# Performance work log

Measured on AMD Instinct MI355X. Metric: run time of the kernel, lower is better.

## Reference

```python
import jax, jax.numpy as jnp
import numpy as np

N = 100000
C_IN, C_OUT = 128, 64
BN_EPS = 1e-5
SLOPE = 0.01  # torch LeakyReLU default


def setup_inputs() -> dict:
    key = jax.random.key(0)
    ks = jax.random.split(key, 12)

    def w(k, K, cin, cout):
        return jax.random.normal(k, (K, cin, cout), jnp.float32) / np.sqrt(K * cin)

    x_feats = jax.random.normal(ks[0], (N, C_IN), jnp.float32)
    skip_feats = jax.random.normal(ks[1], (N, C_OUT), jnp.float32)
    W1 = w(ks[2], 27, C_IN, C_OUT)
    Wt = w(ks[3], 27, C_OUT, C_OUT)
    W2 = w(ks[4], 9, C_OUT, C_OUT)
    W3 = w(ks[5], 9, C_OUT, C_OUT)
    W4 = w(ks[6], 27, C_OUT, C_OUT)
    # bn[l] = (gamma, beta, running_mean, running_var) for BN layer l
    gamma = 1.0 + 0.01 * jax.random.normal(ks[7], (4, C_OUT), jnp.float32)
    beta = 0.01 * jax.random.normal(ks[8], (4, C_OUT), jnp.float32)
    mean = 0.1 * jax.random.normal(ks[9], (4, C_OUT), jnp.float32)
    var = jax.random.uniform(ks[10], (4, C_OUT), jnp.float32, 0.5, 1.5)
    bn = jnp.stack([gamma, beta, mean, var], axis=1)  # [4, 4, C_OUT]

    nk = jax.random.split(ks[11], 5)
    nbr1 = jax.random.randint(nk[0], (27, N), 0, N, jnp.int64)
    nbrt = jax.random.randint(nk[1], (27, N), 0, N, jnp.int64)
    nbr2 = jax.random.randint(nk[2], (9, N), 0, N, jnp.int64)
    nbr3 = jax.random.randint(nk[3], (9, N), 0, N, jnp.int64)
    nbr4 = jax.random.randint(nk[4], (27, N), 0, N, jnp.int64)
    return dict(x_feats=x_feats, skip_feats=skip_feats, W1=W1, Wt=Wt, W2=W2,
                W3=W3, W4=W4, bn=bn, nbr1=nbr1, nbrt=nbrt, nbr2=nbr2,
                nbr3=nbr3, nbr4=nbr4)


def sparse_conv(feats, W, nbr):
    """Gather-GEMM-accumulate sparse conv.

    feats: [N, Cin]; W: [K, Cin, Cout]; nbr: [K, N] neighbor index per tap.
    out[i] = sum_k feats[nbr[k, i]] @ W[k]
    """
    acc0 = jnp.zeros((feats.shape[0], W.shape[-1]), feats.dtype)

    def step(acc, wn):
        w_k, idx_k = wn
        return acc + feats[idx_k] @ w_k, None

    out, _ = jax.lax.scan(step, acc0, (W, nbr))
    return out


def bn_lrelu(x, p):
    gamma, beta, mean, var = p[0], p[1], p[2], p[3]
    y = (x - mean) * jax.lax.rsqrt(var + BN_EPS) * gamma + beta
    return jnp.where(y >= 0, y, SLOPE * y)


def reference(x_feats, skip_feats, W1, Wt, W2, W3, W4, bn,
              nbr1, nbrt, nbr2, nbr3, nbr4):
    # up_block: conv3x3x3 + BN + LeakyReLU, then transposed conv (no BN/act)
    h = bn_lrelu(sparse_conv(x_feats, W1, nbr1), bn[0])
    h = sparse_conv(h, Wt, nbrt)
    h = h + skip_feats  # out.feats += skip.feats
    # conv_x3: three conv blocks
    h = bn_lrelu(sparse_conv(h, W2, nbr2), bn[1])
    h = bn_lrelu(sparse_conv(h, W3, nbr3), bn[2])
    h = bn_lrelu(sparse_conv(h, W4, nbr4), bn[3])
    return h
```

## Files before the change

kernel.cpp:

```cpp
#include <hip/hip_runtime.h>
#include <stdint.h>


typedef __bf16 bf16x8 __attribute__((ext_vector_type(8)));
typedef float f32x16 __attribute__((ext_vector_type(16)));

__device__ __forceinline__ uint16_t f2bf(float f) {
    uint32_t u = __builtin_bit_cast(uint32_t, f);
    u = (u + 0x7fffu + ((u >> 16) & 1u)) >> 16;
    return (uint16_t)u;
}

__device__ __forceinline__ bf16x8 ldb8(const uint16_t* p) {
    return __builtin_bit_cast(bf16x8, *reinterpret_cast<const uint4*>(p));
}

__global__ void convert_x(const float* __restrict__ in, uint16_t* __restrict__ out, int n8) {
    int t = blockIdx.x * blockDim.x + threadIdx.x;
    if (t >= n8) return;
    const float4* p = reinterpret_cast<const float4*>(in) + 2 * (size_t)t;
    float4 f0 = p[0], f1 = p[1];
    uint32_t w0 = (uint32_t)f2bf(f0.x) | ((uint32_t)f2bf(f0.y) << 16);
    uint32_t w1 = (uint32_t)f2bf(f0.z) | ((uint32_t)f2bf(f0.w) << 16);
    uint32_t w2 = (uint32_t)f2bf(f1.x) | ((uint32_t)f2bf(f1.y) << 16);
    uint32_t w3 = (uint32_t)f2bf(f1.z) | ((uint32_t)f2bf(f1.w) << 16);
    uint4 v; v.x = w0; v.y = w1; v.z = w2; v.w = w3;
    *reinterpret_cast<uint4*>(out + 8 * (size_t)t) = v;
}

__global__ void pack_weights(const float* __restrict__ w1, const float* __restrict__ wt,
                             const float* __restrict__ w2, const float* __restrict__ w3,
                             const float* __restrict__ w4, const float* __restrict__ bn,
                             uint16_t* __restrict__ p1, uint16_t* __restrict__ pt,
                             uint16_t* __restrict__ p2, uint16_t* __restrict__ p3,
                             uint16_t* __restrict__ p4, float* __restrict__ bnps) {
    int w = blockIdx.y;
    int t = blockIdx.x * blockDim.x + threadIdx.x;
    if (w == 5) {
        if (t < 256) {
            int l = t >> 6, c = t & 63;
            float g = bn[(l * 4 + 0) * 64 + c];
            float b = bn[(l * 4 + 1) * 64 + c];
            float m = bn[(l * 4 + 2) * 64 + c];
            float v = bn[(l * 4 + 3) * 64 + c];
            float sc = g * rsqrtf(v + 1e-5f);
            bnps[(l * 2 + 0) * 64 + c] = sc;
            bnps[(l * 2 + 1) * 64 + c] = b - m * sc;
        }
        return;
    }
    const float* src; uint16_t* dst; int K, CIN;
    switch (w) {
        case 0:  src = w1; dst = p1; K = 27; CIN = 128; break;
        case 1:  src = wt; dst = pt; K = 27; CIN = 64;  break;
        case 2:  src = w2; dst = p2; K = 9;  CIN = 64;  break;
        case 3:  src = w3; dst = p3; K = 9;  CIN = 64;  break;
        default: src = w4; dst = p4; K = 27; CIN = 64;  break;
    }
    int S = CIN / 16;
    int F = K * S * 2 * 64;
    if (t >= F) return;
    int lane = t & 63;
    int r = t >> 6;
    int nt = r & 1; r >>= 1;
    int s = r % S;
    int k = r / S;
    int c = nt * 32 + (lane & 31);
    int cib = s * 16 + (lane >> 5) * 8;
    #pragma unroll
    for (int j = 0; j < 8; ++j)
        dst[(size_t)t * 8 + j] = f2bf(src[((size_t)k * CIN + cib + j) * 64 + c]);
}

template <int CIN, int MODE>
__global__ __launch_bounds__(64)
void conv_layer(const uint16_t* __restrict__ feats,
                const uint16_t* __restrict__ wf,
                const int* __restrict__ nbr,
                const int K, const int npts,
                const float* __restrict__ bnp,
                const float* __restrict__ skip,
                uint16_t* __restrict__ outb,
                float* __restrict__ outf) {
    constexpr int S = CIN / 16;
    const int lane = threadIdx.x;
    const int l31  = lane & 31;
    const int hi   = lane >> 5;
    const int base = blockIdx.x * 64;
    const int r0 = base + l31;
    const int r1 = r0 + 32;
    const int g0 = min(r0, npts - 1);
    const int g1 = min(r1, npts - 1);

    f32x16 acc00 = {0,0,0,0,0,0,0,0,0,0,0,0,0,0,0,0};
    f32x16 acc01 = {0,0,0,0,0,0,0,0,0,0,0,0,0,0,0,0};
    f32x16 acc10 = {0,0,0,0,0,0,0,0,0,0,0,0,0,0,0,0};
    f32x16 acc11 = {0,0,0,0,0,0,0,0,0,0,0,0,0,0,0,0};

    for (int k = 0; k < K; ++k) {
        const int i0 = nbr[(size_t)k * npts + g0];
        const int i1 = nbr[(size_t)k * npts + g1];
        const uint16_t* a0p = feats + (size_t)i0 * CIN + hi * 8;
        const uint16_t* a1p = feats + (size_t)i1 * CIN + hi * 8;
        const uint16_t* bp  = wf + (size_t)k * (S * 1024) + lane * 8;
        #pragma unroll
        for (int s = 0; s < S; ++s) {
            bf16x8 a0 = ldb8(a0p + s * 16);
            bf16x8 a1 = ldb8(a1p + s * 16);
            bf16x8 b0 = ldb8(bp + s * 1024);
            bf16x8 b1 = ldb8(bp + s * 1024 + 512);
            acc00 = __builtin_amdgcn_mfma_f32_32x32x16_bf16(a0, b0, acc00, 0, 0, 0);
            acc01 = __builtin_amdgcn_mfma_f32_32x32x16_bf16(a0, b1, acc01, 0, 0, 0);
            acc10 = __builtin_amdgcn_mfma_f32_32x32x16_bf16(a1, b0, acc10, 0, 0, 0);
            acc11 = __builtin_amdgcn_mfma_f32_32x32x16_bf16(a1, b1, acc11, 0, 0, 0);
        }
    }

    const int c0 = l31, c1 = 32 + l31;
    float sc0 = 0.f, sh0 = 0.f, sc1 = 0.f, sh1 = 0.f;
    if (MODE != 1) {
        sc0 = bnp[c0]; sh0 = bnp[64 + c0];
        sc1 = bnp[c1]; sh1 = bnp[64 + c1];
    }
    #pragma unroll
    for (int reg = 0; reg < 16; ++reg) {
        const int row = (reg & 3) + 8 * (reg >> 2) + 4 * hi;
        const int gr0 = base + row;
        const int gr1 = base + 32 + row;
        float v00 = acc00[reg], v01 = acc01[reg];
        float v10 = acc10[reg], v11 = acc11[reg];
        if (MODE != 1) {
            v00 = v00 * sc0 + sh0; v00 = v00 >= 0.f ? v00 : 0.01f * v00;
            v01 = v01 * sc1 + sh1; v01 = v01 >= 0.f ? v01 : 0.01f * v01;
            v10 = v10 * sc0 + sh0; v10 = v10 >= 0.f ? v10 : 0.01f * v10;
            v11 = v11 * sc1 + sh1; v11 = v11 >= 0.f ? v11 : 0.01f * v11;
        }
        if (gr0 < npts) {
            if (MODE == 1) { v00 += skip[(size_t)gr0 * 64 + c0]; v01 += skip[(size_t)gr0 * 64 + c1]; }
            if (MODE == 2) {
                outf[(size_t)gr0 * 64 + c0] = v00; outf[(size_t)gr0 * 64 + c1] = v01;
            } else {
                outb[(size_t)gr0 * 64 + c0] = f2bf(v00); outb[(size_t)gr0 * 64 + c1] = f2bf(v01);
            }
        }
        if (gr1 < npts) {
            if (MODE == 1) { v10 += skip[(size_t)gr1 * 64 + c0]; v11 += skip[(size_t)gr1 * 64 + c1]; }
            if (MODE == 2) {
                outf[(size_t)gr1 * 64 + c0] = v10; outf[(size_t)gr1 * 64 + c1] = v11;
            } else {
                outb[(size_t)gr1 * 64 + c0] = f2bf(v10); outb[(size_t)gr1 * 64 + c1] = f2bf(v11);
            }
        }
    }
}

extern "C" void kernel_launch(void* const* d_in, const int* in_sizes, int n_in,
                              void* d_out, int out_size, void* d_ws, size_t ws_size,
                              hipStream_t stream) {
    const int N = in_sizes[0] / 128;
    const float* x    = (const float*)d_in[0];
    const float* skip = (const float*)d_in[1];
    const float* W1   = (const float*)d_in[2];
    const float* Wt   = (const float*)d_in[3];
    const float* W2   = (const float*)d_in[4];
    const float* W3   = (const float*)d_in[5];
    const float* W4   = (const float*)d_in[6];
    const float* bn   = (const float*)d_in[7];
    const int* nbr1   = (const int*)d_in[8];
    const int* nbrt   = (const int*)d_in[9];
    const int* nbr2   = (const int*)d_in[10];
    const int* nbr3   = (const int*)d_in[11];
    const int* nbr4   = (const int*)d_in[12];

    uint8_t* ws = (uint8_t*)d_ws;
    size_t off = 0;
    auto carve = [&](size_t bytes) -> void* {
        void* p = ws + off;
        off += (bytes + 255) & ~(size_t)255;
        return p;
    };
    uint16_t* xb  = (uint16_t*)carve((size_t)N * 128 * 2);
    uint16_t* hA  = (uint16_t*)carve((size_t)N * 64 * 2);
    uint16_t* hB  = (uint16_t*)carve((size_t)N * 64 * 2);
    uint16_t* p1  = (uint16_t*)carve((size_t)27 * 128 * 64 * 2);
    uint16_t* pt  = (uint16_t*)carve((size_t)27 * 64 * 64 * 2);
    uint16_t* p2  = (uint16_t*)carve((size_t)9 * 64 * 64 * 2);
    uint16_t* p3  = (uint16_t*)carve((size_t)9 * 64 * 64 * 2);
    uint16_t* p4  = (uint16_t*)carve((size_t)27 * 64 * 64 * 2);
    float*    bnp = (float*)carve((size_t)4 * 2 * 64 * 4);

    const int n8 = N * 16;
    convert_x<<<(n8 + 255) / 256, 256, 0, stream>>>(x, xb, n8);
    pack_weights<<<dim3(108, 6), 256, 0, stream>>>(W1, Wt, W2, W3, W4, bn,
                                                   p1, pt, p2, p3, p4, bnp);

    const int grid = (N + 63) / 64;
    conv_layer<128, 0><<<grid, 64, 0, stream>>>(xb, p1, nbr1, 27, N, bnp + 0,   nullptr, hA, nullptr);
    conv_layer<64,  1><<<grid, 64, 0, stream>>>(hA, pt, nbrt, 27, N, nullptr,   skip,    hB, nullptr);
    conv_layer<64,  0><<<grid, 64, 0, stream>>>(hB, p2, nbr2, 9,  N, bnp + 128, nullptr, hA, nullptr);
    conv_layer<64,  0><<<grid, 64, 0, stream>>>(hA, p3, nbr3, 9,  N, bnp + 256, nullptr, hB, nullptr);
    conv_layer<64,  2><<<grid, 64, 0, stream>>>(hB, p4, nbr4, 27, N, bnp + 384, nullptr, nullptr, (float*)d_out);
}
```

Before: 536.4 us.

## Split conv tiles to 32 rows per wave, 4 waves per block, prefetch neighbor indices

Each wave now computes a 32-row by 64-channel tile instead of 64 rows, with four waves packed into a 256-thread block, halving accumulator registers and doubling wave count. The tap count K becomes a template parameter, so all neighbor indices for the row are loaded up front into registers before the MFMA loop, taking the index load latency off the per-tap path. In exchange, each weight fragment is reused across half as many rows, so weight-load traffic per output roughly doubles. The larger index array also raises register pressure for K=27.

After: 557.7 us. 1.04x slower.

```diff
diff --git a/kernel.cpp b/kernel.cpp
--- a/kernel.cpp
+++ b/kernel.cpp
@@ -72,47 +72,42 @@
         dst[(size_t)t * 8 + j] = f2bf(src[((size_t)k * CIN + cib + j) * 64 + c]);
 }
 
-template <int CIN, int MODE>
-__global__ __launch_bounds__(64)
+template <int CIN, int K, int MODE>
+__global__ __launch_bounds__(256)
 void conv_layer(const uint16_t* __restrict__ feats,
                 const uint16_t* __restrict__ wf,
                 const int* __restrict__ nbr,
-                const int K, const int npts,
+                const int npts,
                 const float* __restrict__ bnp,
                 const float* __restrict__ skip,
                 uint16_t* __restrict__ outb,
                 float* __restrict__ outf) {
     constexpr int S = CIN / 16;
-    const int lane = threadIdx.x;
+    const int lane = threadIdx.x & 63;
+    const int wave = threadIdx.x >> 6;
     const int l31  = lane & 31;
     const int hi   = lane >> 5;
-    const int base = blockIdx.x * 64;
-    const int r0 = base + l31;
-    const int r1 = r0 + 32;
-    const int g0 = min(r0, npts - 1);
-    const int g1 = min(r1, npts - 1);
+    const int base = (blockIdx.x * 4 + wave) * 32;
+    const int g    = min(base + l31, npts - 1);
 
-    f32x16 acc00 = {0,0,0,0,0,0,0,0,0,0,0,0,0,0,0,0};
-    f32x16 acc01 = {0,0,0,0,0,0,0,0,0,0,0,0,0,0,0,0};
-    f32x16 acc10 = {0,0,0,0,0,0,0,0,0,0,0,0,0,0,0,0};
-    f32x16 acc11 = {0,0,0,0,0,0,0,0,0,0,0,0,0,0,0,0};
+    int idx[K];
+    #pragma unroll
+    for (int k = 0; k < K; ++k) idx[k] = nbr[(size_t)k * npts + g];
 
+    f32x16 acc0 = {0,0,0,0,0,0,0,0,0,0,0,0,0,0,0,0};
+    f32x16 acc1 = {0,0,0,0,0,0,0,0,0,0,0,0,0,0,0,0};
+
+    #pragma unroll 3
     for (int k = 0; k < K; ++k) {
-        const int i0 = nbr[(size_t)k * npts + g0];
-        const int i1 = nbr[(size_t)k * npts + g1];
-        const uint16_t* a0p = feats + (size_t)i0 * CIN + hi * 8;
-        const uint16_t* a1p = feats + (size_t)i1 * CIN + hi * 8;
-        const uint16_t* bp  = wf + (size_t)k * (S * 1024) + lane * 8;
+        const uint16_t* ap = feats + (size_t)idx[k] * CIN + hi * 8;
+        const uint16_t* bp = wf + (size_t)k * (S * 1024) + lane * 8;
         #pragma unroll
         for (int s = 0; s < S; ++s) {
-            bf16x8 a0 = ldb8(a0p + s * 16);
-            bf16x8 a1 = ldb8(a1p + s * 16);
+            bf16x8 a  = ldb8(ap + s * 16);
             bf16x8 b0 = ldb8(bp + s * 1024);
             bf16x8 b1 = ldb8(bp + s * 1024 + 512);
-            acc00 = __builtin_amdgcn_mfma_f32_32x32x16_bf16(a0, b0, acc00, 0, 0, 0);
-            acc01 = __builtin_amdgcn_mfma_f32_32x32x16_bf16(a0, b1, acc01, 0, 0, 0);
-            acc10 = __builtin_amdgcn_mfma_f32_32x32x16_bf16(a1, b0, acc10, 0, 0, 0);
-            acc11 = __builtin_amdgcn_mfma_f32_32x32x16_bf16(a1, b1, acc11, 0, 0, 0);
+            acc0 = __builtin_amdgcn_mfma_f32_32x32x16_bf16(a, b0, acc0, 0, 0, 0);
+            acc1 = __builtin_amdgcn_mfma_f32_32x32x16_bf16(a, b1, acc1, 0, 0, 0);
         }
     }
 
@@ -125,31 +120,22 @@
     #pragma unroll
     for (int reg = 0; reg < 16; ++reg) {
         const int row = (reg & 3) + 8 * (reg >> 2) + 4 * hi;
-        const int gr0 = base + row;
-        const int gr1 = base + 32 + row;
-        float v00 = acc00[reg], v01 = acc01[reg];
-        float v10 = acc10[reg], v11 = acc11[reg];
+        const int gr = base + row;
+        if (gr >= npts) continue;
+        float v0 = acc0[reg], v1 = acc1[reg];
         if (MODE != 1) {
-            v00 = v00 * sc0 + sh0; v00 = v00 >= 0.f ? v00 : 0.01f * v00;
-            v01 = v01 * sc1 + sh1; v01 = v01 >= 0.f ? v01 : 0.01f * v01;
-            v10 = v10 * sc0 + sh0; v10 = v10 >= 0.f ? v10 : 0.01f * v10;
-            v11 = v11 * sc1 + sh1; v11 = v11 >= 0.f ? v11 : 0.01f * v11;
+            v0 = v0 * sc0 + sh0; v0 = v0 >= 0.f ? v0 : 0.01f * v0;
+            v1 = v1 * sc1 + sh1; v1 = v1 >= 0.f ? v1 : 0.01f * v1;
+        } else {
+            v0 += skip[(size_t)gr * 64 + c0];
+            v1 += skip[(size_t)gr * 64 + c1];
         }
-        if (gr0 < npts) {
-            if (MODE == 1) { v00 += skip[(size_t)gr0 * 64 + c0]; v01 += skip[(size_t)gr0 * 64 + c1]; }
-            if (MODE == 2) {
-                outf[(size_t)gr0 * 64 + c0] = v00; outf[(size_t)gr0 * 64 + c1] = v01;
-            } else {
-                outb[(size_t)gr0 * 64 + c0] = f2bf(v00); outb[(size_t)gr0 * 64 + c1] = f2bf(v01);
-            }
-        }
-        if (gr1 < npts) {
-            if (MODE == 1) { v10 += skip[(size_t)gr1 * 64 + c0]; v11 += skip[(size_t)gr1 * 64 + c1]; }
-            if (MODE == 2) {
-                outf[(size_t)gr1 * 64 + c0] = v10; outf[(size_t)gr1 * 64 + c1] = v11;
-            } else {
-                outb[(size_t)gr1 * 64 + c0] = f2bf(v10); outb[(size_t)gr1 * 64 + c1] = f2bf(v11);
-            }
+        if (MODE == 2) {
+            outf[(size_t)gr * 64 + c0] = v0;
+            outf[(size_t)gr * 64 + c1] = v1;
+        } else {
+            outb[(size_t)gr * 64 + c0] = f2bf(v0);
+            outb[(size_t)gr * 64 + c1] = f2bf(v1);
         }
     }
 }
@@ -194,10 +180,10 @@
     pack_weights<<<dim3(108, 6), 256, 0, stream>>>(W1, Wt, W2, W3, W4, bn,
                                                    p1, pt, p2, p3, p4, bnp);
 
-    const int grid = (N + 63) / 64;
-    conv_layer<128, 0><<<grid, 64, 0, stream>>>(xb, p1, nbr1, 27, N, bnp + 0,   nullptr, hA, nullptr);
-    conv_layer<64,  1><<<grid, 64, 0, stream>>>(hA, pt, nbrt, 27, N, nullptr,   skip,    hB, nullptr);
-    conv_layer<64,  0><<<grid, 64, 0, stream>>>(hB, p2, nbr2, 9,  N, bnp + 128, nullptr, hA, nullptr);
-    conv_layer<64,  0><<<grid, 64, 0, stream>>>(hA, p3, nbr3, 9,  N, bnp + 256, nullptr, hB, nullptr);
-    conv_layer<64,  2><<<grid, 64, 0, stream>>>(hB, p4, nbr4, 27, N, bnp + 384, nullptr, nullptr, (float*)d_out);
+    const int grid = (N + 127) / 128;
+    conv_layer<128, 27, 0><<<grid, 256, 0, stream>>>(xb, p1, nbr1, N, bnp + 0,   nullptr, hA, nullptr);
+    conv_layer<64,  27, 1><<<grid, 256, 0, stream>>>(hA, pt, nbrt, N, nullptr,   skip,    hB, nullptr);
+    conv_layer<64,  9,  0><<<grid, 256, 0, stream>>>(hB, p2, nbr2, N, bnp + 128, nullptr, hA, nullptr);
+    conv_layer<64,  9,  0><<<grid, 256, 0, stream>>>(hA, p3, nbr3, N, bnp + 256, nullptr, hB, nullptr);
+    conv_layer<64,  27, 2><<<grid, 256, 0, stream>>>(hB, p4, nbr4, N, bnp + 384, nullptr, nullptr, (float*)d_out);
 }
```

## Fuse conversion, packing and five conv layers into one cooperative kernel

Applied to the files above, without the earlier changes.

Merges the input conversion, weight packing and all five sparse conv layers into a single cooperative kernel, with a grid-wide sync between stages. Each block loops over tiles with a grid stride. The goal is to remove the per-kernel launch gaps and the tail drain between the seven separate launches. In exchange it adds grid-sync cost, and the fused kernel may need more registers, which could lower occupancy or make the cooperative launch fail. If the launch fails, it falls back to the original multi-kernel path.

New measurement: 1.739 ms. 224% more time.

```diff
diff --git a/kernel.cpp b/kernel.cpp
--- a/kernel.cpp
+++ b/kernel.cpp
@@ -1,5 +1,8 @@
 #include <hip/hip_runtime.h>
+#include <hip/hip_cooperative_groups.h>
 #include <stdint.h>
+
+namespace cg = cooperative_groups;
 
 
 typedef __bf16 bf16x8 __attribute__((ext_vector_type(8)));
@@ -15,9 +18,9 @@
     return __builtin_bit_cast(bf16x8, *reinterpret_cast<const uint4*>(p));
 }
 
-__global__ void convert_x(const float* __restrict__ in, uint16_t* __restrict__ out, int n8) {
-    int t = blockIdx.x * blockDim.x + threadIdx.x;
-    if (t >= n8) return;
+
+__device__ __forceinline__ void convert_body(const float* __restrict__ in,
+                                             uint16_t* __restrict__ out, int t) {
     const float4* p = reinterpret_cast<const float4*>(in) + 2 * (size_t)t;
     float4 f0 = p[0], f1 = p[1];
     uint32_t w0 = (uint32_t)f2bf(f0.x) | ((uint32_t)f2bf(f0.y) << 16);
@@ -28,65 +31,47 @@
     *reinterpret_cast<uint4*>(out + 8 * (size_t)t) = v;
 }
 
-__global__ void pack_weights(const float* __restrict__ w1, const float* __restrict__ wt,
-                             const float* __restrict__ w2, const float* __restrict__ w3,
-                             const float* __restrict__ w4, const float* __restrict__ bn,
-                             uint16_t* __restrict__ p1, uint16_t* __restrict__ pt,
-                             uint16_t* __restrict__ p2, uint16_t* __restrict__ p3,
-                             uint16_t* __restrict__ p4, float* __restrict__ bnps) {
-    int w = blockIdx.y;
-    int t = blockIdx.x * blockDim.x + threadIdx.x;
-    if (w == 5) {
-        if (t < 256) {
-            int l = t >> 6, c = t & 63;
-            float g = bn[(l * 4 + 0) * 64 + c];
-            float b = bn[(l * 4 + 1) * 64 + c];
-            float m = bn[(l * 4 + 2) * 64 + c];
-            float v = bn[(l * 4 + 3) * 64 + c];
-            float sc = g * rsqrtf(v + 1e-5f);
-            bnps[(l * 2 + 0) * 64 + c] = sc;
-            bnps[(l * 2 + 1) * 64 + c] = b - m * sc;
-        }
-        return;
-    }
-    const float* src; uint16_t* dst; int K, CIN;
-    switch (w) {
-        case 0:  src = w1; dst = p1; K = 27; CIN = 128; break;
-        case 1:  src = wt; dst = pt; K = 27; CIN = 64;  break;
-        case 2:  src = w2; dst = p2; K = 9;  CIN = 64;  break;
-        case 3:  src = w3; dst = p3; K = 9;  CIN = 64;  break;
-        default: src = w4; dst = p4; K = 27; CIN = 64;  break;
-    }
+__device__ __forceinline__ void pack_body(const float* __restrict__ src,
+                                          uint16_t* __restrict__ dst,
+                                          int CIN, int t) {
     int S = CIN / 16;
-    int F = K * S * 2 * 64;
-    if (t >= F) return;
-    int lane = t & 63;
+    int l = t & 63;
     int r = t >> 6;
     int nt = r & 1; r >>= 1;
     int s = r % S;
     int k = r / S;
-    int c = nt * 32 + (lane & 31);
-    int cib = s * 16 + (lane >> 5) * 8;
+    int c = nt * 32 + (l & 31);
+    int cib = s * 16 + (l >> 5) * 8;
     #pragma unroll
     for (int j = 0; j < 8; ++j)
         dst[(size_t)t * 8 + j] = f2bf(src[((size_t)k * CIN + cib + j) * 64 + c]);
 }
 
+__device__ __forceinline__ void bn_body(const float* __restrict__ bn,
+                                        float* __restrict__ bnps, int t) {
+    int l = t >> 6, c = t & 63;
+    float g = bn[(l * 4 + 0) * 64 + c];
+    float b = bn[(l * 4 + 1) * 64 + c];
+    float m = bn[(l * 4 + 2) * 64 + c];
+    float v = bn[(l * 4 + 3) * 64 + c];
+    float sc = g * rsqrtf(v + 1e-5f);
+    bnps[(l * 2 + 0) * 64 + c] = sc;
+    bnps[(l * 2 + 1) * 64 + c] = b - m * sc;
+}
+
 template <int CIN, int MODE>
-__global__ __launch_bounds__(64)
-void conv_layer(const uint16_t* __restrict__ feats,
-                const uint16_t* __restrict__ wf,
-                const int* __restrict__ nbr,
-                const int K, const int npts,
-                const float* __restrict__ bnp,
-                const float* __restrict__ skip,
-                uint16_t* __restrict__ outb,
-                float* __restrict__ outf) {
+__device__ void conv_tile(int base, int lane,
+                          const uint16_t* __restrict__ feats,
+                          const uint16_t* __restrict__ wf,
+                          const int* __restrict__ nbr,
+                          const int K, const int npts,
+                          const float* __restrict__ bnp,
+                          const float* __restrict__ skip,
+                          uint16_t* __restrict__ outb,
+                          float* __restrict__ outf) {
     constexpr int S = CIN / 16;
-    const int lane = threadIdx.x;
-    const int l31  = lane & 31;
-    const int hi   = lane >> 5;
-    const int base = blockIdx.x * 64;
+    const int l31 = lane & 31;
+    const int hi  = lane >> 5;
     const int r0 = base + l31;
     const int r1 = r0 + 32;
     const int g0 = min(r0, npts - 1);
@@ -154,23 +139,85 @@
     }
 }
 
+struct UPParams {
+    const float* x; const float* skip;
+    const float* W1; const float* Wt; const float* W2; const float* W3; const float* W4;
+    const float* bn;
+    const int* nbr1; const int* nbrt; const int* nbr2; const int* nbr3; const int* nbr4;
+    uint16_t* xb; uint16_t* hA; uint16_t* hB;
+    uint16_t* p1; uint16_t* pt; uint16_t* p2; uint16_t* p3; uint16_t* p4;
+    float* bnp; float* out;
+    int N; int n8; int ntiles;
+};
+
+__global__ __launch_bounds__(64)
+void fused_upblock(UPParams P) {
+    cg::grid_group grid = cg::this_grid();
+    const int lane = threadIdx.x;
+    const int gthreads = gridDim.x * 64;
+    const int gt0 = blockIdx.x * 64 + lane;
+
+    for (int t = gt0; t < P.n8; t += gthreads) convert_body(P.x, P.xb, t);
+    for (int t = gt0; t < 27 * 8 * 2 * 64; t += gthreads) pack_body(P.W1, P.p1, 128, t);
+    for (int t = gt0; t < 27 * 4 * 2 * 64; t += gthreads) pack_body(P.Wt, P.pt, 64, t);
+    for (int t = gt0; t < 9 * 4 * 2 * 64;  t += gthreads) pack_body(P.W2, P.p2, 64, t);
+    for (int t = gt0; t < 9 * 4 * 2 * 64;  t += gthreads) pack_body(P.W3, P.p3, 64, t);
+    for (int t = gt0; t < 27 * 4 * 2 * 64; t += gthreads) pack_body(P.W4, P.p4, 64, t);
+    for (int t = gt0; t < 256; t += gthreads) bn_body(P.bn, P.bnp, t);
+
+    __threadfence(); grid.sync(); __threadfence();
+
+    for (int tile = blockIdx.x; tile < P.ntiles; tile += gridDim.x)
+        conv_tile<128, 0>(tile * 64, lane, P.xb, P.p1, P.nbr1, 27, P.N, P.bnp, nullptr, P.hA, nullptr);
+    __threadfence(); grid.sync(); __threadfence();
+
+    for (int tile = blockIdx.x; tile < P.ntiles; tile += gridDim.x)
+        conv_tile<64, 1>(tile * 64, lane, P.hA, P.pt, P.nbrt, 27, P.N, nullptr, P.skip, P.hB, nullptr);
+    __threadfence(); grid.sync(); __threadfence();
+
+    for (int tile = blockIdx.x; tile < P.ntiles; tile += gridDim.x)
+        conv_tile<64, 0>(tile * 64, lane, P.hB, P.p2, P.nbr2, 9, P.N, P.bnp + 128, nullptr, P.hA, nullptr);
+    __threadfence(); grid.sync(); __threadfence();
+
+    for (int tile = blockIdx.x; tile < P.ntiles; tile += gridDim.x)
+        conv_tile<64, 0>(tile * 64, lane, P.hA, P.p3, P.nbr3, 9, P.N, P.bnp + 256, nullptr, P.hB, nullptr);
+    __threadfence(); grid.sync(); __threadfence();
+
+    for (int tile = blockIdx.x; tile < P.ntiles; tile += gridDim.x)
+        conv_tile<64, 2>(tile * 64, lane, P.hB, P.p4, P.nbr4, 27, P.N, P.bnp + 384, nullptr, nullptr, P.out);
+}
+
+__global__ void convert_x_g(const float* __restrict__ in, uint16_t* __restrict__ out, int n8) {
+    int t = blockIdx.x * blockDim.x + threadIdx.x;
+    if (t < n8) convert_body(in, out, t);
+}
+
+__global__ void pack_weights_g(UPParams P) {
+    int w = blockIdx.y;
+    int t = blockIdx.x * blockDim.x + threadIdx.x;
+    switch (w) {
+        case 0: if (t < 27 * 8 * 2 * 64) pack_body(P.W1, P.p1, 128, t); break;
+        case 1: if (t < 27 * 4 * 2 * 64) pack_body(P.Wt, P.pt, 64, t); break;
+        case 2: if (t < 9 * 4 * 2 * 64)  pack_body(P.W2, P.p2, 64, t); break;
+        case 3: if (t < 9 * 4 * 2 * 64)  pack_body(P.W3, P.p3, 64, t); break;
+        case 4: if (t < 27 * 4 * 2 * 64) pack_body(P.W4, P.p4, 64, t); break;
+        default: if (t < 256) bn_body(P.bn, P.bnp, t); break;
+    }
+}
+
+template <int CIN, int MODE>
+__global__ __launch_bounds__(64)
+void conv_layer_g(const uint16_t* __restrict__ feats, const uint16_t* __restrict__ wf,
+                  const int* __restrict__ nbr, const int K, const int npts,
+                  const float* __restrict__ bnp, const float* __restrict__ skip,
+                  uint16_t* __restrict__ outb, float* __restrict__ outf) {
+    conv_tile<CIN, MODE>(blockIdx.x * 64, threadIdx.x, feats, wf, nbr, K, npts, bnp, skip, outb, outf);
+}
+
 extern "C" void kernel_launch(void* const* d_in, const int* in_sizes, int n_in,
                               void* d_out, int out_size, void* d_ws, size_t ws_size,
                               hipStream_t stream) {
     const int N = in_sizes[0] / 128;
-    const float* x    = (const float*)d_in[0];
-    const float* skip = (const float*)d_in[1];
-    const float* W1   = (const float*)d_in[2];
-    const float* Wt   = (const float*)d_in[3];
-    const float* W2   = (const float*)d_in[4];
-    const float* W3   = (const float*)d_in[5];
-    const float* W4   = (const float*)d_in[6];
-    const float* bn   = (const float*)d_in[7];
-    const int* nbr1   = (const int*)d_in[8];
-    const int* nbrt   = (const int*)d_in[9];
-    const int* nbr2   = (const int*)d_in[10];
-    const int* nbr3   = (const int*)d_in[11];
-    const int* nbr4   = (const int*)d_in[12];
 
     uint8_t* ws = (uint8_t*)d_ws;
     size_t off = 0;
@@ -179,25 +226,47 @@
         off += (bytes + 255) & ~(size_t)255;
         return p;
     };
-    uint16_t* xb  = (uint16_t*)carve((size_t)N * 128 * 2);
-    uint16_t* hA  = (uint16_t*)carve((size_t)N * 64 * 2);
-    uint16_t* hB  = (uint16_t*)carve((size_t)N * 64 * 2);
-    uint16_t* p1  = (uint16_t*)carve((size_t)27 * 128 * 64 * 2);
-    uint16_t* pt  = (uint16_t*)carve((size_t)27 * 64 * 64 * 2);
-    uint16_t* p2  = (uint16_t*)carve((size_t)9 * 64 * 64 * 2);
-    uint16_t* p3  = (uint16_t*)carve((size_t)9 * 64 * 64 * 2);
-    uint16_t* p4  = (uint16_t*)carve((size_t)27 * 64 * 64 * 2);
-    float*    bnp = (float*)carve((size_t)4 * 2 * 64 * 4);
-
-    const int n8 = N * 16;
-    convert_x<<<(n8 + 255) / 256, 256, 0, stream>>>(x, xb, n8);
-    pack_weights<<<dim3(108, 6), 256, 0, stream>>>(W1, Wt, W2, W3, W4, bn,
-                                                   p1, pt, p2, p3, p4, bnp);
-
-    const int grid = (N + 63) / 64;
-    conv_layer<128, 0><<<grid, 64, 0, stream>>>(xb, p1, nbr1, 27, N, bnp + 0,   nullptr, hA, nullptr);
-    conv_layer<64,  1><<<grid, 64, 0, stream>>>(hA, pt, nbrt, 27, N, nullptr,   skip,    hB, nullptr);
-    conv_layer<64,  0><<<grid, 64, 0, stream>>>(hB, p2, nbr2, 9,  N, bnp + 128, nullptr, hA, nullptr);
-    conv_layer<64,  0><<<grid, 64, 0, stream>>>(hA, p3, nbr3, 9,  N, bnp + 256, nullptr, hB, nullptr);
-    conv_layer<64,  2><<<grid, 64, 0, stream>>>(hB, p4, nbr4, 27, N, bnp + 384, nullptr, nullptr, (float*)d_out);
-}
+
+    UPParams P;
+    P.x    = (const float*)d_in[0];
+    P.skip = (const float*)d_in[1];
+    P.W1   = (const float*)d_in[2];
+    P.Wt   = (const float*)d_in[3];
+    P.W2   = (const float*)d_in[4];
+    P.W3   = (const float*)d_in[5];
+    P.W4   = (const float*)d_in[6];
+    P.bn   = (const float*)d_in[7];
+    P.nbr1 = (const int*)d_in[8];
+    P.nbrt = (const int*)d_in[9];
+    P.nbr2 = (const int*)d_in[10];
+    P.nbr3 = (const int*)d_in[11];
+    P.nbr4 = (const int*)d_in[12];
+    P.xb   = (uint16_t*)carve((size_t)N * 128 * 2);
+    P.hA   = (uint16_t*)carve((size_t)N * 64 * 2);
+    P.hB   = (uint16_t*)carve((size_t)N * 64 * 2);
+    P.p1   = (uint16_t*)carve((size_t)27 * 128 * 64 * 2);
+    P.pt   = (uint16_t*)carve((size_t)27 * 64 * 64 * 2);
+    P.p2   = (uint16_t*)carve((size_t)9 * 64 * 64 * 2);
+    P.p3   = (uint16_t*)carve((size_t)9 * 64 * 64 * 2);
+    P.p4   = (uint16_t*)carve((size_t)27 * 64 * 64 * 2);
+    P.bnp  = (float*)carve((size_t)4 * 2 * 64 * 4);
+    P.out  = (float*)d_out;
+    P.N = N;
+    P.n8 = N * 16;
+    P.ntiles = (N + 63) / 64;
+
+    void* kargs[] = { (void*)&P };
+    hipError_t err = hipLaunchCooperativeKernel((const void*)fused_upblock,
+                                                dim3(P.ntiles), dim3(64),
+                                                kargs, 0, stream);
+    if (err != hipSuccess) {
+        convert_x_g<<<(P.n8 + 255) / 256, 256, 0, stream>>>(P.x, P.xb, P.n8);
+        pack_weights_g<<<dim3(108, 6), 256, 0, stream>>>(P);
+        const int grid = P.ntiles;
+        conv_layer_g<128, 0><<<grid, 64, 0, stream>>>(P.xb, P.p1, P.nbr1, 27, N, P.bnp,       nullptr, P.hA, nullptr);
+        conv_layer_g<64,  1><<<grid, 64, 0, stream>>>(P.hA, P.pt, P.nbrt, 27, N, nullptr,     P.skip,  P.hB, nullptr);
+        conv_layer_g<64,  0><<<grid, 64, 0, stream>>>(P.hB, P.p2, P.nbr2, 9,  N, P.bnp + 128, nullptr, P.hA, nullptr);
+        conv_layer_g<64,  0><<<grid, 64, 0, stream>>>(P.hA, P.p3, P.nbr3, 9,  N, P.bnp + 256, nullptr, P.hB, nullptr);
+        conv_layer_g<64,  2><<<grid, 64, 0, stream>>>(P.hB, P.p4, P.nbr4, 27, N, P.bnp + 384, nullptr, nullptr, P.out);
+    }
+}
```

## Stage conv weights in LDS shared by four waves per block

Applied to the files above, without the earlier changes.

Each block now runs four waves, each computing 64 output rows, and cooperatively copies chunks of taps' packed weights into 64KB of shared memory. The waves then read B fragments from LDS instead of global memory. This cuts redundant weight traffic through L2/L1 and makes K a compile-time constant so the tap loops can unroll. In exchange it adds barriers per chunk and uses a large LDS footprint, which can limit blocks per CU and reduce occupancy for this gather-latency-bound kernel.

New measurement: 548.3 us. +2.2%, slower.

```diff
diff --git a/kernel.cpp b/kernel.cpp
--- a/kernel.cpp
+++ b/kernel.cpp
@@ -72,48 +72,74 @@
         dst[(size_t)t * 8 + j] = f2bf(src[((size_t)k * CIN + cib + j) * 64 + c]);
 }
 
-template <int CIN, int MODE>
-__global__ __launch_bounds__(64)
+template <int CIN, int K, int MODE>
+__global__ __launch_bounds__(256)
 void conv_layer(const uint16_t* __restrict__ feats,
                 const uint16_t* __restrict__ wf,
                 const int* __restrict__ nbr,
-                const int K, const int npts,
+                const int npts,
                 const float* __restrict__ bnp,
                 const float* __restrict__ skip,
                 uint16_t* __restrict__ outb,
                 float* __restrict__ outf) {
     constexpr int S = CIN / 16;
-    const int lane = threadIdx.x;
+    constexpr int C = 32 / S;
+    constexpr int NFULL = K / C;
+    constexpr int REM = K % C;
+
+    __shared__ uint16_t Bs[32768];
+
+    const int lane = threadIdx.x & 63;
+    const int wave = threadIdx.x >> 6;
     const int l31  = lane & 31;
     const int hi   = lane >> 5;
-    const int base = blockIdx.x * 64;
-    const int r0 = base + l31;
-    const int r1 = r0 + 32;
-    const int g0 = min(r0, npts - 1);
-    const int g1 = min(r1, npts - 1);
+    const int base = (blockIdx.x * 4 + wave) * 64;
+    const int g0   = min(base + l31, npts - 1);
+    const int g1   = min(base + 32 + l31, npts - 1);
 
     f32x16 acc00 = {0,0,0,0,0,0,0,0,0,0,0,0,0,0,0,0};
     f32x16 acc01 = {0,0,0,0,0,0,0,0,0,0,0,0,0,0,0,0};
     f32x16 acc10 = {0,0,0,0,0,0,0,0,0,0,0,0,0,0,0,0};
     f32x16 acc11 = {0,0,0,0,0,0,0,0,0,0,0,0,0,0,0,0};
 
-    for (int k = 0; k < K; ++k) {
+    auto stage = [&](int k0, int units) {
+        const uint4* gsrc = reinterpret_cast<const uint4*>(wf + (size_t)k0 * (S * 1024));
+        uint4* dst = reinterpret_cast<uint4*>(Bs);
+        for (int u = threadIdx.x; u < units; u += 256) dst[u] = gsrc[u];
+    };
+
+    auto do_tap = [&](int k, int kk) {
         const int i0 = nbr[(size_t)k * npts + g0];
         const int i1 = nbr[(size_t)k * npts + g1];
         const uint16_t* a0p = feats + (size_t)i0 * CIN + hi * 8;
         const uint16_t* a1p = feats + (size_t)i1 * CIN + hi * 8;
-        const uint16_t* bp  = wf + (size_t)k * (S * 1024) + lane * 8;
         #pragma unroll
         for (int s = 0; s < S; ++s) {
             bf16x8 a0 = ldb8(a0p + s * 16);
             bf16x8 a1 = ldb8(a1p + s * 16);
-            bf16x8 b0 = ldb8(bp + s * 1024);
-            bf16x8 b1 = ldb8(bp + s * 1024 + 512);
+            const uint16_t* bp = Bs + ((kk * S + s) * 2) * 512 + lane * 8;
+            bf16x8 b0 = ldb8(bp);
+            bf16x8 b1 = ldb8(bp + 512);
             acc00 = __builtin_amdgcn_mfma_f32_32x32x16_bf16(a0, b0, acc00, 0, 0, 0);
             acc01 = __builtin_amdgcn_mfma_f32_32x32x16_bf16(a0, b1, acc01, 0, 0, 0);
             acc10 = __builtin_amdgcn_mfma_f32_32x32x16_bf16(a1, b0, acc10, 0, 0, 0);
             acc11 = __builtin_amdgcn_mfma_f32_32x32x16_bf16(a1, b1, acc11, 0, 0, 0);
         }
+    };
+
+    for (int c = 0; c < NFULL; ++c) {
+        stage(c * C, C * S * 128);
+        __syncthreads();
+        #pragma unroll
+        for (int kk = 0; kk < C; ++kk) do_tap(c * C + kk, kk);
+        __syncthreads();
+    }
+    if constexpr (REM > 0) {
+        stage(NFULL * C, REM * S * 128);
+        __syncthreads();
+        #pragma unroll
+        for (int kk = 0; kk < REM; ++kk) do_tap(NFULL * C + kk, kk);
+        __syncthreads();
     }
 
     const int c0 = l31, c1 = 32 + l31;
@@ -194,10 +220,10 @@
     pack_weights<<<dim3(108, 6), 256, 0, stream>>>(W1, Wt, W2, W3, W4, bn,
                                                    p1, pt, p2, p3, p4, bnp);
 
-    const int grid = (N + 63) / 64;
-    conv_layer<128, 0><<<grid, 64, 0, stream>>>(xb, p1, nbr1, 27, N, bnp + 0,   nullptr, hA, nullptr);
-    conv_layer<64,  1><<<grid, 64, 0, stream>>>(hA, pt, nbrt, 27, N, nullptr,   skip,    hB, nullptr);
-    conv_layer<64,  0><<<grid, 64, 0, stream>>>(hB, p2, nbr2, 9,  N, bnp + 128, nullptr, hA, nullptr);
-    conv_layer<64,  0><<<grid, 64, 0, stream>>>(hA, p3, nbr3, 9,  N, bnp + 256, nullptr, hB, nullptr);
-    conv_layer<64,  2><<<grid, 64, 0, stream>>>(hB, p4, nbr4, 27, N, bnp + 384, nullptr, nullptr, (float*)d_out);
-}
+    const int grid = (N + 255) / 256;
+    conv_layer<128, 27, 0><<<grid, 256, 0, stream>>>(xb, p1, nbr1, N, bnp + 0,   nullptr, hA, nullptr);
+    conv_layer<64,  27, 1><<<grid, 256, 0, stream>>>(hA, pt, nbrt, N, nullptr,   skip,    hB, nullptr);
+    conv_layer<64,  9,  0><<<grid, 256, 0, stream>>>(hB, p2, nbr2, N, bnp + 128, nullptr, hA, nullptr);
+    conv_layer<64,  9,  0><<<grid, 256, 0, stream>>>(hA, p3, nbr3, N, bnp + 256, nullptr, hB, nullptr);
+    conv_layer<64,  27, 2><<<grid, 256, 0, stream>>>(hB, p4, nbr4, N, bnp + 384, nullptr, nullptr, (float*)d_out);
+}
```
